# Kernel tuning notes

Measured on AMD Instinct MI355X. Metric: run time of the kernel, lower is better.

## Reference

```python
import jax, jax.numpy as jnp
import numpy as np

N_NEURONS = 2048
IN_DIM = 1024
OUT_DIM = 1024
TOKENS = 4096
TIME_STEPS = 3
DENSITY = 0.25


def setup_inputs() -> dict:
    key = jax.random.key(0)
    ks = jax.random.split(key, 10)
    x = jax.random.normal(ks[0], (TOKENS, IN_DIM), dtype=jnp.float32)
    W_in = jax.random.normal(ks[1], (N_NEURONS, IN_DIM), dtype=jnp.float32) * (1.0 / np.sqrt(IN_DIM))
    b_in = jax.random.normal(ks[2], (N_NEURONS,), dtype=jnp.float32) * 0.01
    weights = jax.random.normal(ks[3], (N_NEURONS, N_NEURONS), dtype=jnp.float32) * 0.3
    J = jax.random.normal(ks[4], (N_NEURONS, N_NEURONS), dtype=jnp.float32) * 0.1
    theta = jax.random.uniform(ks[5], (N_NEURONS,), dtype=jnp.float32) * 1.0 + 0.25
    lam = jnp.asarray(0.35, dtype=jnp.float32)
    # connection mask: rand < density, zero diagonal (buffer, fixed)
    m = (jax.random.uniform(ks[6], (N_NEURONS, N_NEURONS)) < DENSITY).astype(jnp.float32)
    mask = m * (1.0 - jnp.eye(N_NEURONS, dtype=jnp.float32))
    noise_raw = jax.random.normal(ks[7], (TIME_STEPS, TOKENS, N_NEURONS), dtype=jnp.float32)
    W_out = jax.random.normal(ks[8], (OUT_DIM, N_NEURONS), dtype=jnp.float32) * (1.0 / np.sqrt(N_NEURONS))
    b_out = jax.random.normal(ks[9], (OUT_DIM,), dtype=jnp.float32) * 0.01
    return {"x": x, "W_in": W_in, "b_in": b_in, "weights": weights, "J": J,
            "theta": theta, "lam": lam, "mask": mask, "noise_raw": noise_raw,
            "W_out": W_out, "b_out": b_out, "time_steps": TIME_STEPS}


def reference(x, W_in, b_in, weights, J, theta, lam, mask, noise_raw, W_out, b_out, time_steps):
    # input projection: [tokens, in_dim] -> [tokens, n]
    state = x @ W_in.T + b_in
    eff_w = weights * mask          # [n, n]
    J_m = J * mask                  # [n, n]
    T = jnp.abs(jnp.sin(2.0 * theta))  # temperature [n]
    for t in range(time_steps):
        signal = state @ eff_w                     # [tokens, n]
        s = jnp.tanh(state)
        # einsum('bi,ij,bj->bj', s, J_m, s) == (s @ J_m) * s
        delta = (s @ J_m) * s                      # [tokens, n]
        noise = noise_raw[t] * T * 0.1             # [tokens, n]
        state = jnp.tanh(signal + lam * delta + noise)
    return state @ W_out.T + b_out
```

## Files before the change

### kernel.cpp

```cpp
#include <hip/hip_runtime.h>
#include <hip/hip_fp16.h>

#define TOKENS 4096
#define NN 2048
#define IN_DIM 1024
#define OUT_DIM 1024
#define TSTEPS 3

typedef _Float16 half8 __attribute__((ext_vector_type(8)));
typedef _Float16 half4 __attribute__((ext_vector_type(4)));
typedef float f32x4 __attribute__((ext_vector_type(4)));

__device__ __forceinline__ void gload_lds16(const void* g, void* l) {
    __builtin_amdgcn_global_load_lds(
        (const __attribute__((address_space(1))) unsigned*)g,
        (__attribute__((address_space(3))) unsigned*)l, 16, 0, 0);
}

#define LGKM(N) asm volatile("s_waitcnt lgkmcnt(" #N ")" ::: "memory")
#define VMCNT(N) asm volatile("s_waitcnt vmcnt(" #N ")" ::: "memory")
#define SCHED0() __builtin_amdgcn_sched_barrier(0)

__global__ __launch_bounds__(512, 2)
void dual_gemm(const _Float16* __restrict__ A0g, const _Float16* __restrict__ B0g,
               _Float16* __restrict__ C0,
               const _Float16* __restrict__ A1g, const _Float16* __restrict__ B1g,
               _Float16* __restrict__ C1)
{
    __shared__ __align__(16) _Float16 lds[2 * 32768];
    const int tid  = threadIdx.x;
    const int wid  = tid >> 6;
    const int lane = tid & 63;

    const int raw  = blockIdx.x;
    const int widx = (raw & 7) * 32 + (raw >> 3);
    const int g    = widx >> 7;
    const int bid  = widx & 127;
    const int by = bid >> 3;
    const int bx = bid & 7;
    const _Float16* __restrict__ A = g ? A1g : A0g;
    const _Float16* __restrict__ B = g ? B1g : B0g;
    _Float16* __restrict__ C = g ? C1 : C0;
    const int brow = by << 8;
    const int bcol = bx << 8;

    const int sr = tid >> 3;
    const int sc = ((tid & 7) ^ (sr & 7)) << 3;
    const _Float16* gA = A + (size_t)(brow + sr) * NN + sc;
    const _Float16* gB = B + (size_t)(bcol + sr) * NN + sc;
    const int ldst = wid << 9;

    auto stA = [&](int T, int h) {
        _Float16* l = lds + (T & 1) * 32768 + h * 8192;
        const _Float16* p = gA + (size_t)(h << 7) * NN + (T << 6);
        gload_lds16(p,           l + ldst);
        gload_lds16(p + 64 * NN, l + 4096 + ldst);
    };
    auto stB = [&](int T, int h) {
        _Float16* l = lds + (T & 1) * 32768 + 16384 + h * 8192;
        const _Float16* p = gB + (size_t)(h << 7) * NN + (T << 6);
        gload_lds16(p,           l + ldst);
        gload_lds16(p + 64 * NN, l + 4096 + ldst);
    };

    const int wr = (wid >> 2) << 7;
    const int wc = (wid & 3) << 6;
    const int lr = lane & 15;
    const int lq = lane >> 4;
    const int x7 = lr & 7;
    const int c0 = (lq ^ x7) << 3;
    const int c1 = ((4 + lq) ^ x7) << 3;
    const int aRow = (wr + lr) << 6;
    const int bRow = 16384 + ((wc + lr) << 6);

    f32x4 acc[8][4];
#pragma unroll
    for (int m = 0; m < 8; ++m)
#pragma unroll
        for (int n = 0; n < 4; ++n) acc[m][n] = (f32x4){0.f, 0.f, 0.f, 0.f};

    half8 af0[4], af1[4], af2[4], af3[4], bf0[4], bf1[4];

    stA(0, 0); stA(0, 1); stB(0, 0); stB(0, 1);
    stA(1, 0); stA(1, 1); stB(1, 0); stB(1, 1);
    VMCNT(8);
    __builtin_amdgcn_s_barrier();
    {
        const _Float16* lb = lds;
#pragma unroll
        for (int m = 0; m < 4; ++m) af0[m] = *(const half8*)&lb[aRow + (m << 10) + c0];
#pragma unroll
        for (int n = 0; n < 4; ++n) bf0[n] = *(const half8*)&lb[bRow + (n << 10) + c0];
    }

    for (int T = 0; T < 32; ++T) {
        const _Float16* lb = lds + (T & 1) * 32768;

#pragma unroll
        for (int m = 0; m < 4; ++m) af1[m] = *(const half8*)&lb[aRow + ((m + 4) << 10) + c0];
        LGKM(4);
        SCHED0();
        __builtin_amdgcn_s_setprio(1);
#pragma unroll
        for (int m = 0; m < 4; ++m)
#pragma unroll
            for (int n = 0; n < 4; ++n)
                acc[m][n] = __builtin_amdgcn_mfma_f32_16x16x32_f16(af0[m], bf0[n], acc[m][n], 0, 0, 0);
        __builtin_amdgcn_s_setprio(0);
        SCHED0();

#pragma unroll
        for (int m = 0; m < 4; ++m) af2[m] = *(const half8*)&lb[aRow + (m << 10) + c1];
#pragma unroll
        for (int n = 0; n < 4; ++n) bf1[n] = *(const half8*)&lb[bRow + (n << 10) + c1];
        LGKM(8);
        SCHED0();
        __builtin_amdgcn_s_setprio(1);
#pragma unroll
        for (int m = 0; m < 4; ++m)
#pragma unroll
            for (int n = 0; n < 4; ++n)
                acc[m + 4][n] = __builtin_amdgcn_mfma_f32_16x16x32_f16(af1[m], bf0[n], acc[m + 4][n], 0, 0, 0);
        __builtin_amdgcn_s_setprio(0);
        SCHED0();

#pragma unroll
        for (int m = 0; m < 4; ++m) af3[m] = *(const half8*)&lb[aRow + ((m + 4) << 10) + c1];
        LGKM(4);
        SCHED0();
        __builtin_amdgcn_s_setprio(1);
#pragma unroll
        for (int m = 0; m < 4; ++m)
#pragma unroll
            for (int n = 0; n < 4; ++n)
                acc[m][n] = __builtin_amdgcn_mfma_f32_16x16x32_f16(af2[m], bf1[n], acc[m][n], 0, 0, 0);
        __builtin_amdgcn_s_setprio(0);
        SCHED0();

        LGKM(0);
        __builtin_amdgcn_s_barrier();
        if (T < 30) { stA(T + 2, 0); stA(T + 2, 1); stB(T + 2, 0); stB(T + 2, 1); }
        if (T < 30) { VMCNT(8); }
        else        { VMCNT(0); }
        __builtin_amdgcn_s_barrier();
        asm volatile("" ::: "memory");

        if (T < 31) {
            const _Float16* ln = lds + ((T + 1) & 1) * 32768;
#pragma unroll
            for (int m = 0; m < 4; ++m) af0[m] = *(const half8*)&ln[aRow + (m << 10) + c0];
#pragma unroll
            for (int n = 0; n < 4; ++n) bf0[n] = *(const half8*)&ln[bRow + (n << 10) + c0];
        }
        SCHED0();
        __builtin_amdgcn_s_setprio(1);
#pragma unroll
        for (int m = 0; m < 4; ++m)
#pragma unroll
            for (int n = 0; n < 4; ++n)
                acc[m + 4][n] = __builtin_amdgcn_mfma_f32_16x16x32_f16(af3[m], bf1[n], acc[m + 4][n], 0, 0, 0);
        __builtin_amdgcn_s_setprio(0);
        SCHED0();
    }

    const int cr = lq << 2;
    const int cc = lane & 15;
#pragma unroll
    for (int m = 0; m < 8; ++m) {
#pragma unroll
        for (int n = 0; n < 4; ++n) {
            const size_t o0 = (size_t)(brow + wr + m * 16 + cr) * NN
                            + (bcol + wc + n * 16 + cc);
#pragma unroll
            for (int j = 0; j < 4; ++j)
                C[o0 + (size_t)j * NN] = (_Float16)acc[m][n][j];
        }
    }
}

template<int EPI>
__global__ __launch_bounds__(256, 2)
void pgemm(const _Float16* __restrict__ A, const _Float16* __restrict__ B,
           float* __restrict__ Cout, const float* __restrict__ bias,
           _Float16* __restrict__ oSta, _Float16* __restrict__ oS,
           int K, int N, int nbxLog2)
{
    __shared__ __align__(16) _Float16 lds[2 * 16384];
    const int tid  = threadIdx.x;
    const int wid  = tid >> 6;
    const int lane = tid & 63;

    const int raw  = blockIdx.x;
    const int cpx  = gridDim.x >> 3;
    const int widx = (raw & 7) * cpx + (raw >> 3);
    const int by = widx >> nbxLog2;
    const int bx = widx & ((1 << nbxLog2) - 1);
    const int brow = by << 7;
    const int bcol = bx << 7;

    const int sr = tid >> 3;
    const int sc = ((tid & 7) ^ (sr & 7)) << 3;
    const _Float16* gA = A + (size_t)(brow + sr) * K + sc;
    const _Float16* gB = B + (size_t)(bcol + sr) * K + sc;
    const int ldst = wid << 9;

    auto stA = [&](int T) {
        _Float16* l = lds + (T & 1) * 16384;
        const _Float16* p = gA + (T << 6);
#pragma unroll
        for (int r = 0; r < 4; ++r)
            gload_lds16(p + (size_t)(r * 32) * K, l + r * 2048 + ldst);
    };
    auto stB = [&](int T) {
        _Float16* l = lds + (T & 1) * 16384 + 8192;
        const _Float16* p = gB + (T << 6);
#pragma unroll
        for (int r = 0; r < 4; ++r)
            gload_lds16(p + (size_t)(r * 32) * K, l + r * 2048 + ldst);
    };

    const int wr = (wid >> 1) << 6;
    const int wc = (wid & 1) << 6;
    const int lr = lane & 15;
    const int lq = lane >> 4;
    const int x7 = lr & 7;
    const int c0 = (lq ^ x7) << 3;
    const int c1 = ((4 + lq) ^ x7) << 3;
    const int aRow = (wr + lr) << 6;
    const int bRow = 8192 + ((wc + lr) << 6);

    f32x4 acc[4][4];
#pragma unroll
    for (int m = 0; m < 4; ++m)
#pragma unroll
        for (int n = 0; n < 4; ++n) acc[m][n] = (f32x4){0.f, 0.f, 0.f, 0.f};

    half8 af0[4], af1[4], bf0[4], bf1[4];
    const int NT = K >> 6;

    stA(0); stB(0); stA(1); stB(1);
    VMCNT(8);
    __builtin_amdgcn_s_barrier();
    {
        const _Float16* lb = lds;
#pragma unroll
        for (int m = 0; m < 4; ++m) af0[m] = *(const half8*)&lb[aRow + (m << 10) + c0];
#pragma unroll
        for (int n = 0; n < 4; ++n) bf0[n] = *(const half8*)&lb[bRow + (n << 10) + c0];
    }

    for (int T = 0; T < NT; ++T) {
        const _Float16* lb = lds + (T & 1) * 16384;

#pragma unroll
        for (int m = 0; m < 4; ++m) af1[m] = *(const half8*)&lb[aRow + (m << 10) + c1];
#pragma unroll
        for (int n = 0; n < 4; ++n) bf1[n] = *(const half8*)&lb[bRow + (n << 10) + c1];
        LGKM(8);
        SCHED0();
        __builtin_amdgcn_s_setprio(1);
#pragma unroll
        for (int m = 0; m < 4; ++m)
#pragma unroll
            for (int n = 0; n < 4; ++n)
                acc[m][n] = __builtin_amdgcn_mfma_f32_16x16x32_f16(af0[m], bf0[n], acc[m][n], 0, 0, 0);
        __builtin_amdgcn_s_setprio(0);
        SCHED0();

        LGKM(0);
        __builtin_amdgcn_s_barrier();
        if (T < NT - 2) { stA(T + 2); stB(T + 2); VMCNT(8); }
        else if (T == NT - 2) { VMCNT(0); }
        __builtin_amdgcn_s_barrier();
        asm volatile("" ::: "memory");

        if (T < NT - 1) {
            const _Float16* ln = lds + ((T + 1) & 1) * 16384;
#pragma unroll
            for (int m = 0; m < 4; ++m) af0[m] = *(const half8*)&ln[aRow + (m << 10) + c0];
#pragma unroll
            for (int n = 0; n < 4; ++n) bf0[n] = *(const half8*)&ln[bRow + (n << 10) + c0];
        }
        SCHED0();
        __builtin_amdgcn_s_setprio(1);
#pragma unroll
        for (int m = 0; m < 4; ++m)
#pragma unroll
            for (int n = 0; n < 4; ++n)
                acc[m][n] = __builtin_amdgcn_mfma_f32_16x16x32_f16(af1[m], bf1[n], acc[m][n], 0, 0, 0);
        __builtin_amdgcn_s_setprio(0);
        SCHED0();
    }

    const int cr = lq << 2;
    const int cc = lane & 15;
#pragma unroll
    for (int m = 0; m < 4; ++m) {
#pragma unroll
        for (int n = 0; n < 4; ++n) {
            const int ccol = bcol + wc + n * 16 + cc;
#pragma unroll
            for (int j = 0; j < 4; ++j) {
                const int crow = brow + wr + m * 16 + cr + j;
                float v = acc[m][n][j] + bias[ccol];
                const size_t o = (size_t)crow * N + ccol;
                if (EPI == 1) {
                    oSta[o] = (_Float16)v;
                    oS[o] = (_Float16)tanhf(v);
                } else {
                    Cout[o] = v;
                }
            }
        }
    }
}

__global__ void cvt_f16(const float* __restrict__ in, _Float16* __restrict__ out, int n4) {
    int i = blockIdx.x * blockDim.x + threadIdx.x;
    if (i < n4) {
        f32x4 v = *(const f32x4*)&in[(size_t)i * 4];
        half4 h;
        h[0] = (_Float16)v[0]; h[1] = (_Float16)v[1];
        h[2] = (_Float16)v[2]; h[3] = (_Float16)v[3];
        *(half4*)&out[(size_t)i * 4] = h;
    }
}

__global__ void transmul2(const float* __restrict__ W, const float* __restrict__ J,
                          const float* __restrict__ Mk,
                          _Float16* __restrict__ effT, _Float16* __restrict__ JmT) {
    __shared__ float tw[32][33];
    __shared__ float tj[32][33];
    const int bx = blockIdx.x * 32, by = blockIdx.y * 32;
    const int tx = threadIdx.x, ty0 = threadIdx.y;
#pragma unroll
    for (int r = 0; r < 4; ++r) {
        int ty = ty0 + r * 8;
        size_t idx = (size_t)(by + ty) * NN + bx + tx;
        float mv = Mk[idx];
        tw[ty][tx] = W[idx] * mv;
        tj[ty][tx] = J[idx] * mv;
    }
    __syncthreads();
#pragma unroll
    for (int r = 0; r < 4; ++r) {
        int ty = ty0 + r * 8;
        size_t o = (size_t)(bx + ty) * NN + by + tx;
        effT[o] = (_Float16)tw[tx][ty];
        JmT[o]  = (_Float16)tj[tx][ty];
    }
}

__global__ void tsc_kernel(const float* __restrict__ theta, float* __restrict__ Tsc) {
    int i = blockIdx.x * blockDim.x + threadIdx.x;
    if (i < NN) Tsc[i] = fabsf(sinf(2.0f * theta[i])) * 0.1f;
}

__global__ void step_kernel(const _Float16* __restrict__ signalH, const _Float16* __restrict__ sJH,
                            const float* __restrict__ noise, const float* __restrict__ Tsc,
                            const float* __restrict__ lamp,
                            _Float16* __restrict__ stateH, _Float16* __restrict__ sH) {
    const int i4 = blockIdx.x * blockDim.x + threadIdx.x;
    const float lam = lamp[0];
    const size_t base = (size_t)i4 * 4;
    half4 sg = *(const half4*)&signalH[base];
    half4 dj = *(const half4*)&sJH[base];
    f32x4 nz = *(const f32x4*)&noise[base];
    const int col4 = (int)(base & (NN - 1));
    f32x4 tv = *(const f32x4*)&Tsc[col4];
    half4 so = *(const half4*)&sH[base];
    half4 hs, hn;
#pragma unroll
    for (int j = 0; j < 4; ++j) {
        float s = (float)so[j];
        float arg = (float)sg[j] + lam * ((float)dj[j] * s) + nz[j] * tv[j];
        float st = tanhf(arg);
        hs[j] = (_Float16)st;
        hn[j] = (_Float16)tanhf(st);
    }
    *(half4*)&stateH[base] = hs;
    *(half4*)&sH[base] = hn;
}

extern "C" void kernel_launch(void* const* d_in, const int* in_sizes, int n_in,
                              void* d_out, int out_size, void* d_ws, size_t ws_size,
                              hipStream_t stream) {
    const float* x       = (const float*)d_in[0];
    const float* W_in    = (const float*)d_in[1];
    const float* b_in    = (const float*)d_in[2];
    const float* weights = (const float*)d_in[3];
    const float* Jmat    = (const float*)d_in[4];
    const float* theta   = (const float*)d_in[5];
    const float* lam     = (const float*)d_in[6];
    const float* mask    = (const float*)d_in[7];
    const float* noise   = (const float*)d_in[8];
    const float* W_out   = (const float*)d_in[9];
    const float* b_out   = (const float*)d_in[10];
    float* out = (float*)d_out;

    char* w = (char*)d_ws;
    auto alloc = [&](size_t b) { char* p = w; w += (b + 255) & ~(size_t)255; return p; };
    _Float16* xh      = (_Float16*)alloc((size_t)TOKENS * IN_DIM * 2);
    _Float16* WinH    = (_Float16*)alloc((size_t)NN * IN_DIM * 2);
    _Float16* WoutH   = (_Float16*)alloc((size_t)OUT_DIM * NN * 2);
    _Float16* effT    = (_Float16*)alloc((size_t)NN * NN * 2);
    _Float16* JmT     = (_Float16*)alloc((size_t)NN * NN * 2);
    _Float16* stateH  = (_Float16*)alloc((size_t)TOKENS * NN * 2);
    _Float16* sH      = (_Float16*)alloc((size_t)TOKENS * NN * 2);
    _Float16* signalH = (_Float16*)alloc((size_t)TOKENS * NN * 2);
    _Float16* sJH     = (_Float16*)alloc((size_t)TOKENS * NN * 2);
    float* Tsc        = (float*)alloc((size_t)NN * 4);

    cvt_f16<<<TOKENS * IN_DIM / 4 / 256, 256, 0, stream>>>(x, xh, TOKENS * IN_DIM / 4);
    cvt_f16<<<NN * IN_DIM / 4 / 256, 256, 0, stream>>>(W_in, WinH, NN * IN_DIM / 4);
    cvt_f16<<<OUT_DIM * NN / 4 / 256, 256, 0, stream>>>(W_out, WoutH, OUT_DIM * NN / 4);
    transmul2<<<dim3(NN / 32, NN / 32), dim3(32, 8), 0, stream>>>(weights, Jmat, mask, effT, JmT);
    tsc_kernel<<<NN / 256, 256, 0, stream>>>(theta, Tsc);

    pgemm<1><<<(TOKENS / 128) * (NN / 128), 256, 0, stream>>>(
        xh, WinH, nullptr, b_in, stateH, sH, IN_DIM, NN, 4);

    for (int t = 0; t < TSTEPS; ++t) {
        dual_gemm<<<256, 512, 0, stream>>>(stateH, effT, signalH, sH, JmT, sJH);
        step_kernel<<<TOKENS * NN / 4 / 256, 256, 0, stream>>>(
            signalH, sJH, noise + (size_t)t * TOKENS * NN, Tsc, lam, stateH, sH);
    }

    pgemm<2><<<(TOKENS / 128) * (OUT_DIM / 128), 256, 0, stream>>>(
        stateH, WoutH, out, b_out, nullptr, nullptr, NN, OUT_DIM, 3);
}
```

Baseline: 341.1 us.

## Restructure dual_gemm LDS fragment loads and merge three fp16 conversion kernels

```diff
diff --git a/kernel.cpp b/kernel.cpp
--- a/kernel.cpp
+++ b/kernel.cpp
@@ -79,25 +79,52 @@
 #pragma unroll
         for (int n = 0; n < 4; ++n) acc[m][n] = (f32x4){0.f, 0.f, 0.f, 0.f};
 
-    half8 af0[4], af1[4], af2[4], af3[4], bf0[4], bf1[4];
+    half8 a0[8], a1[8], b0[4], b1[4];
 
     stA(0, 0); stA(0, 1); stB(0, 0); stB(0, 1);
     stA(1, 0); stA(1, 1); stB(1, 0); stB(1, 1);
     VMCNT(8);
     __builtin_amdgcn_s_barrier();
-    {
-        const _Float16* lb = lds;
-#pragma unroll
-        for (int m = 0; m < 4; ++m) af0[m] = *(const half8*)&lb[aRow + (m << 10) + c0];
-#pragma unroll
-        for (int n = 0; n < 4; ++n) bf0[n] = *(const half8*)&lb[bRow + (n << 10) + c0];
-    }
+    asm volatile("" ::: "memory");
 
     for (int T = 0; T < 32; ++T) {
         const _Float16* lb = lds + (T & 1) * 32768;
 
 #pragma unroll
-        for (int m = 0; m < 4; ++m) af1[m] = *(const half8*)&lb[aRow + ((m + 4) << 10) + c0];
+        for (int m = 0; m < 4; ++m) a0[m] = *(const half8*)&lb[aRow + (m << 10) + c0];
+#pragma unroll
+        for (int n = 0; n < 4; ++n) b0[n] = *(const half8*)&lb[bRow + (n << 10) + c0];
+#pragma unroll
+        for (int m = 4; m < 8; ++m) a0[m] = *(const half8*)&lb[aRow + (m << 10) + c0];
+#pragma unroll
+        for (int m = 0; m < 4; ++m) a1[m] = *(const half8*)&lb[aRow + (m << 10) + c1];
+#pragma unroll
+        for (int n = 0; n < 4; ++n) b1[n] = *(const half8*)&lb[bRow + (n << 10) + c1];
+#pragma unroll
+        for (int m = 4; m < 8; ++m) a1[m] = *(const half8*)&lb[aRow + (m << 10) + c1];
+
+        LGKM(15);
+        SCHED0();
+        __builtin_amdgcn_s_setprio(1);
+#pragma unroll
+        for (int m = 0; m < 4; ++m)
+#pragma unroll
+            for (int n = 0; n < 4; ++n)
+                acc[m][n] = __builtin_amdgcn_mfma_f32_16x16x32_f16(a0[m], b0[n], acc[m][n], 0, 0, 0);
+        __builtin_amdgcn_s_setprio(0);
+        SCHED0();
+
+        LGKM(12);
+        SCHED0();
+        __builtin_amdgcn_s_setprio(1);
+#pragma unroll
+        for (int m = 0; m < 4; ++m)
+#pragma unroll
+            for (int n = 0; n < 4; ++n)
+                acc[m + 4][n] = __builtin_amdgcn_mfma_f32_16x16x32_f16(a0[m + 4], b0[n], acc[m + 4][n], 0, 0, 0);
+        __builtin_amdgcn_s_setprio(0);
+        SCHED0();
+
         LGKM(4);
         SCHED0();
         __builtin_amdgcn_s_setprio(1);
@@ -105,35 +132,7 @@
         for (int m = 0; m < 4; ++m)
 #pragma unroll
             for (int n = 0; n < 4; ++n)
-                acc[m][n] = __builtin_amdgcn_mfma_f32_16x16x32_f16(af0[m], bf0[n], acc[m][n], 0, 0, 0);
-        __builtin_amdgcn_s_setprio(0);
-        SCHED0();
-
-#pragma unroll
-        for (int m = 0; m < 4; ++m) af2[m] = *(const half8*)&lb[aRow + (m << 10) + c1];
-#pragma unroll
-        for (int n = 0; n < 4; ++n) bf1[n] = *(const half8*)&lb[bRow + (n << 10) + c1];
-        LGKM(8);
-        SCHED0();
-        __builtin_amdgcn_s_setprio(1);
-#pragma unroll
-        for (int m = 0; m < 4; ++m)
-#pragma unroll
-            for (int n = 0; n < 4; ++n)
-                acc[m + 4][n] = __builtin_amdgcn_mfma_f32_16x16x32_f16(af1[m], bf0[n], acc[m + 4][n], 0, 0, 0);
-        __builtin_amdgcn_s_setprio(0);
-        SCHED0();
-
-#pragma unroll
-        for (int m = 0; m < 4; ++m) af3[m] = *(const half8*)&lb[aRow + ((m + 4) << 10) + c1];
-        LGKM(4);
-        SCHED0();
-        __builtin_amdgcn_s_setprio(1);
-#pragma unroll
-        for (int m = 0; m < 4; ++m)
-#pragma unroll
-            for (int n = 0; n < 4; ++n)
-                acc[m][n] = __builtin_amdgcn_mfma_f32_16x16x32_f16(af2[m], bf1[n], acc[m][n], 0, 0, 0);
+                acc[m][n] = __builtin_amdgcn_mfma_f32_16x16x32_f16(a1[m], b1[n], acc[m][n], 0, 0, 0);
         __builtin_amdgcn_s_setprio(0);
         SCHED0();
 
@@ -145,20 +144,12 @@
         __builtin_amdgcn_s_barrier();
         asm volatile("" ::: "memory");
 
-        if (T < 31) {
-            const _Float16* ln = lds + ((T + 1) & 1) * 32768;
-#pragma unroll
-            for (int m = 0; m < 4; ++m) af0[m] = *(const half8*)&ln[aRow + (m << 10) + c0];
-#pragma unroll
-            for (int n = 0; n < 4; ++n) bf0[n] = *(const half8*)&ln[bRow + (n << 10) + c0];
-        }
-        SCHED0();
-        __builtin_amdgcn_s_setprio(1);
-#pragma unroll
-        for (int m = 0; m < 4; ++m)
-#pragma unroll
-            for (int n = 0; n < 4; ++n)
-                acc[m + 4][n] = __builtin_amdgcn_mfma_f32_16x16x32_f16(af3[m], bf1[n], acc[m + 4][n], 0, 0, 0);
+        __builtin_amdgcn_s_setprio(1);
+#pragma unroll
+        for (int m = 0; m < 4; ++m)
+#pragma unroll
+            for (int n = 0; n < 4; ++n)
+                acc[m + 4][n] = __builtin_amdgcn_mfma_f32_16x16x32_f16(a1[m + 4], b1[n], acc[m + 4][n], 0, 0, 0);
         __builtin_amdgcn_s_setprio(0);
         SCHED0();
     }
@@ -315,15 +306,19 @@
     }
 }
 
-__global__ void cvt_f16(const float* __restrict__ in, _Float16* __restrict__ out, int n4) {
+__global__ void cvt3(const float* __restrict__ s0, _Float16* __restrict__ d0, int n0,
+                     const float* __restrict__ s1, _Float16* __restrict__ d1, int n1,
+                     const float* __restrict__ s2, _Float16* __restrict__ d2) {
     int i = blockIdx.x * blockDim.x + threadIdx.x;
-    if (i < n4) {
-        f32x4 v = *(const f32x4*)&in[(size_t)i * 4];
-        half4 h;
-        h[0] = (_Float16)v[0]; h[1] = (_Float16)v[1];
-        h[2] = (_Float16)v[2]; h[3] = (_Float16)v[3];
-        *(half4*)&out[(size_t)i * 4] = h;
-    }
+    const float* src; _Float16* dst; int k;
+    if (i < n0)            { src = s0; dst = d0; k = i; }
+    else if (i < n0 + n1)  { src = s1; dst = d1; k = i - n0; }
+    else                   { src = s2; dst = d2; k = i - n0 - n1; }
+    f32x4 v = *(const f32x4*)&src[(size_t)k * 4];
+    half4 h;
+    h[0] = (_Float16)v[0]; h[1] = (_Float16)v[1];
+    h[2] = (_Float16)v[2]; h[3] = (_Float16)v[3];
+    *(half4*)&dst[(size_t)k * 4] = h;
 }
 
 __global__ void transmul2(const float* __restrict__ W, const float* __restrict__ J,
@@ -411,9 +406,10 @@
     _Float16* sJH     = (_Float16*)alloc((size_t)TOKENS * NN * 2);
     float* Tsc        = (float*)alloc((size_t)NN * 4);
 
-    cvt_f16<<<TOKENS * IN_DIM / 4 / 256, 256, 0, stream>>>(x, xh, TOKENS * IN_DIM / 4);
-    cvt_f16<<<NN * IN_DIM / 4 / 256, 256, 0, stream>>>(W_in, WinH, NN * IN_DIM / 4);
-    cvt_f16<<<OUT_DIM * NN / 4 / 256, 256, 0, stream>>>(W_out, WoutH, OUT_DIM * NN / 4);
+    const int n0 = TOKENS * IN_DIM / 4;
+    const int n1 = NN * IN_DIM / 4;
+    const int n2 = OUT_DIM * NN / 4;
+    cvt3<<<(n0 + n1 + n2) / 256, 256, 0, stream>>>(x, xh, n0, W_in, WinH, n1, W_out, WoutH);
     transmul2<<<dim3(NN / 32, NN / 32), dim3(32, 8), 0, stream>>>(weights, Jmat, mask, effT, JmT);
     tsc_kernel<<<NN / 256, 256, 0, stream>>>(theta, Tsc);
 
```

After: 339.9 us. Within noise of the previous version (-0.3%).
